# Optimization experiments

Measured on AMD Instinct MI355X. Metric: run time of the kernel, lower is better.

The kernel has to match this reference:

```python
import jax, jax.numpy as jnp
import numpy as np

DIM = 1024
H = 16
DH = DIM // H  # 64
B = 2
T = 2048
LEFT, RIGHT = 128, 128  # attention_window
CAUSAL = True
SCALE = 1.0 / float(np.sqrt(DH))


def rotate_half(x):
    x1, x2 = jnp.split(x, 2, axis=-1)
    return jnp.concatenate((-x2, x1), axis=-1)


def apply_rotary_pos_emb(pos, t):
    # pos: [b, t, dh] -> [b, 1, t, dh]; t: [b, h, t, dh]
    pos = pos[:, None]
    return t * jnp.cos(pos) + rotate_half(t) * jnp.sin(pos)


def setup_inputs() -> dict:
    key = jax.random.key(0)
    ks = jax.random.split(key, 6)
    s = 1.0 / np.sqrt(DIM)
    x = jax.random.normal(ks[0], (B, T, DIM), dtype=jnp.float32)
    attention_mask = jnp.ones((T, T), dtype=bool)
    rotary_emb = jax.random.normal(ks[1], (B, T, DH), dtype=jnp.float32)
    Wq = jax.random.normal(ks[2], (DIM, DIM), dtype=jnp.float32) * s
    Wk = jax.random.normal(ks[3], (DIM, DIM), dtype=jnp.float32) * s
    Wv = jax.random.normal(ks[4], (DIM, DIM), dtype=jnp.float32) * s
    Wo = jax.random.normal(ks[5], (DIM, DIM), dtype=jnp.float32) * s
    return {"x": x, "attention_mask": attention_mask, "rotary_emb": rotary_emb,
            "Wq": Wq, "Wk": Wk, "Wv": Wv, "Wo": Wo}


def _build_mask(attention_mask):
    # i = key/column index, j = query/row index (matches torch code)
    i = jnp.arange(T)[None, :]
    j = jnp.arange(T)[:, None]
    mask = (i >= j - LEFT) & (i <= j + RIGHT)  # sliding window
    if CAUSAL:
        mask = mask & (i <= j)  # tril
    return attention_mask & mask  # [T, T]


def reference(x, attention_mask, rotary_emb, Wq, Wk, Wv, Wo):
    b, t, d = x.shape
    # QKV projections (nn.Linear: x @ W.T), split heads: b t (h dh) -> b h t dh
    def proj(W):
        return (x @ W.T).reshape(b, t, H, DH).transpose(0, 2, 1, 3)
    q, k, v = proj(Wq), proj(Wk), proj(Wv)
    q = apply_rotary_pos_emb(rotary_emb, q)
    k = apply_rotary_pos_emb(rotary_emb, k)
    mask = _build_mask(attention_mask)  # [T, T]
    scores = jnp.einsum('bhqd,bhkd->bhqk', q, k) * SCALE
    neg = jnp.asarray(-1e9, scores.dtype)
    scores = jnp.where(mask, scores, neg)
    attn = jax.nn.softmax(scores, axis=-1)
    out = jnp.einsum('bhqk,bhkd->bhqd', attn, v)
    out = out.transpose(0, 2, 1, 3).reshape(b, t, d)  # b h t dh -> b t (h dh)
    return out @ Wo.T
```

## Files before the change

kernel.cpp:

```cpp
#include <hip/hip_runtime.h>
#include <hip/hip_bf16.h>
#include <cstdint>

#define DIMD 1024
#define NH 16
#define DHD 64
#define BB 2
#define TT 2048
#define MROWS (BB * TT)

typedef unsigned short u16;
typedef unsigned int u32;
typedef __attribute__((ext_vector_type(8))) __bf16 bf16x8;
typedef __attribute__((ext_vector_type(4))) float f32x4;

__device__ __forceinline__ float bf2f(u16 u) {
    union { unsigned int i; float f; } v; v.i = ((unsigned int)u) << 16; return v.f;
}
__device__ __forceinline__ u16 f2bf(float f) {
    union { float f; unsigned int i; } v; v.f = f;
    unsigned int u = v.i;
    unsigned int r = (u + 0x7fffu + ((u >> 16) & 1u)) >> 16;
    return (u16)r;
}
__device__ __forceinline__ int4 pack8(const float4& a, const float4& b) {
    union { int4 v; u16 u[8]; } t;
    t.u[0] = f2bf(a.x); t.u[1] = f2bf(a.y); t.u[2] = f2bf(a.z); t.u[3] = f2bf(a.w);
    t.u[4] = f2bf(b.x); t.u[5] = f2bf(b.y); t.u[6] = f2bf(b.z); t.u[7] = f2bf(b.w);
    return t.v;
}
__device__ __forceinline__ void gl_lds16(const u16* g, u16* l) {
    __builtin_amdgcn_global_load_lds(
        (const __attribute__((address_space(1))) u32*)g,
        (__attribute__((address_space(3))) u32*)l, 16, 0, 0);
}

__global__ __launch_bounds__(256) void convert_all(const float* __restrict__ x,
                                                   const float* __restrict__ Wq,
                                                   const float* __restrict__ Wk,
                                                   const float* __restrict__ Wv,
                                                   const float* __restrict__ Wo,
                                                   u16* __restrict__ xb,
                                                   u16* __restrict__ wqkv,
                                                   u16* __restrict__ wob) {
    int t = blockIdx.x * 256 + threadIdx.x;
    const float* src; u16* dst; int rel;
    if (t < 524288)      { src = x;  dst = xb;             rel = t; }
    else if (t < 655360) { src = Wq; dst = wqkv;           rel = t - 524288; }
    else if (t < 786432) { src = Wk; dst = wqkv + 1048576; rel = t - 655360; }
    else if (t < 917504) { src = Wv; dst = wqkv + 2097152; rel = t - 786432; }
    else                 { src = Wo; dst = wob;            rel = t - 917504; }
    size_t e = (size_t)rel * 8;
    float4 a = *(const float4*)(src + e);
    float4 b = *(const float4*)(src + e + 4);
    *(int4*)(dst + e) = pack8(a, b);
}

__global__ __launch_bounds__(256) void gemm_qkv(const u16* __restrict__ xb,
                                                const u16* __restrict__ wqkv,
                                                u16* __restrict__ qb,
                                                u16* __restrict__ kb,
                                                u16* __restrict__ vb,
                                                const float* __restrict__ rot) {
    constexpr int Kd = 1024;
    __shared__ u16 As[128 * 32];
    __shared__ u16 Bs[128 * 32];

    const int tid  = threadIdx.x;
    const int lane = tid & 63;
    const int w    = tid >> 6;
    const int m0   = blockIdx.y * 128;
    const int n0   = blockIdx.x * 128;

    const u16* Ag = xb   + (size_t)(m0 + 32 * w + (lane >> 2)) * Kd + (lane & 3) * 8;
    const u16* Bg = wqkv + (size_t)(n0 + 32 * w + (lane & 63) / 4) * Kd + (lane & 3) * 8;
    u16* Al0 = &As[(32 * w) * 32];
    u16* Al1 = &As[(32 * w + 16) * 32];
    u16* Bl0 = &Bs[(32 * w) * 32];
    u16* Bl1 = &Bs[(32 * w + 16) * 32];

    const int r16  = lane & 15;
    const int quad = lane >> 4;
    const int q8   = quad * 8;
    const int wm   = (w >> 1) * 64;
    const int wn   = (w & 1) * 64;

    f32x4 acc[4][4];
#pragma unroll
    for (int i = 0; i < 4; i++)
#pragma unroll
        for (int j = 0; j < 4; j++) acc[i][j] = f32x4{0.f, 0.f, 0.f, 0.f};

    for (int k0 = 0; k0 < Kd; k0 += 32) {
        __syncthreads();
        gl_lds16(Ag + k0, Al0);
        gl_lds16(Ag + 16 * Kd + k0, Al1);
        gl_lds16(Bg + k0, Bl0);
        gl_lds16(Bg + 16 * Kd + k0, Bl1);
        __syncthreads();

        bf16x8 af[4], bfr[4];
#pragma unroll
        for (int i = 0; i < 4; i++)
            af[i] = *(const bf16x8*)&As[(wm + i * 16 + r16) * 32 + q8];
#pragma unroll
        for (int j = 0; j < 4; j++)
            bfr[j] = *(const bf16x8*)&Bs[(wn + j * 16 + r16) * 32 + q8];
#pragma unroll
        for (int mi = 0; mi < 4; mi++)
#pragma unroll
            for (int ni = 0; ni < 4; ni++)
                acc[mi][ni] = __builtin_amdgcn_mfma_f32_16x16x32_bf16(
                    af[mi], bfr[ni], acc[mi][ni], 0, 0, 0);
    }

    const int wsel = n0 >> 10;
    const int nloc = (n0 & 1023) + wn;
    u16* C = (wsel == 0) ? qb : (wsel == 1) ? kb : vb;

    if (wsel < 2) {
#pragma unroll
        for (int mi = 0; mi < 4; mi++)
#pragma unroll
            for (int r = 0; r < 4; r++) {
                int row = m0 + wm + mi * 16 + quad * 4 + r;
#pragma unroll
                for (int ni = 0; ni < 2; ni++) {
                    int d = ni * 16 + r16;
                    float s0, c0, s1, c1;
                    __sincosf(rot[row * DHD + d], &s0, &c0);
                    __sincosf(rot[row * DHD + d + 32], &s1, &c1);
                    float x0 = acc[mi][ni][r], x1 = acc[mi][ni + 2][r];
                    C[(size_t)row * DIMD + nloc + d]      = f2bf(x0 * c0 - x1 * s0);
                    C[(size_t)row * DIMD + nloc + d + 32] = f2bf(x1 * c1 + x0 * s1);
                }
            }
    } else {
#pragma unroll
        for (int mi = 0; mi < 4; mi++)
#pragma unroll
            for (int ni = 0; ni < 4; ni++)
#pragma unroll
                for (int r = 0; r < 4; r++) {
                    int row = m0 + wm + mi * 16 + quad * 4 + r;
                    C[(size_t)row * DIMD + nloc + ni * 16 + r16] = f2bf(acc[mi][ni][r]);
                }
    }
}

__global__ __launch_bounds__(256) void gemm_out(const u16* __restrict__ A,
                                                const u16* __restrict__ Wb,
                                                float* __restrict__ C) {
    constexpr int Kd = 1024, Nd = 1024;
    __shared__ u16 As[64 * 32];
    __shared__ u16 Bs[128 * 32];

    const int tid  = threadIdx.x;
    const int lane = tid & 63;
    const int w    = tid >> 6;
    const int m0   = blockIdx.y * 64;
    const int n0   = blockIdx.x * 128;

    const u16* Ag = A  + (size_t)(m0 + 16 * w + (lane >> 2)) * Kd + (lane & 3) * 8;
    const u16* Bg = Wb + (size_t)(n0 + 32 * w + (lane >> 2)) * Kd + (lane & 3) * 8;
    u16* Al  = &As[(16 * w) * 32];
    u16* Bl0 = &Bs[(32 * w) * 32];
    u16* Bl1 = &Bs[(32 * w + 16) * 32];

    const int r16  = lane & 15;
    const int quad = lane >> 4;
    const int q8   = quad * 8;
    const int cb   = (w >> 1) * 64 + (w & 1) * 16;

    f32x4 acc[4][2];
#pragma unroll
    for (int i = 0; i < 4; i++)
#pragma unroll
        for (int j = 0; j < 2; j++) acc[i][j] = f32x4{0.f, 0.f, 0.f, 0.f};

    for (int k0 = 0; k0 < Kd; k0 += 32) {
        __syncthreads();
        gl_lds16(Ag + k0, Al);
        gl_lds16(Bg + k0, Bl0);
        gl_lds16(Bg + 16 * Kd + k0, Bl1);
        __syncthreads();

        bf16x8 af[4], bfr[2];
#pragma unroll
        for (int i = 0; i < 4; i++)
            af[i] = *(const bf16x8*)&As[(i * 16 + r16) * 32 + q8];
#pragma unroll
        for (int j = 0; j < 2; j++)
            bfr[j] = *(const bf16x8*)&Bs[(cb + j * 32 + r16) * 32 + q8];
#pragma unroll
        for (int mi = 0; mi < 4; mi++)
#pragma unroll
            for (int ni = 0; ni < 2; ni++)
                acc[mi][ni] = __builtin_amdgcn_mfma_f32_16x16x32_bf16(
                    af[mi], bfr[ni], acc[mi][ni], 0, 0, 0);
    }

#pragma unroll
    for (int mi = 0; mi < 4; mi++)
#pragma unroll
        for (int j = 0; j < 2; j++)
#pragma unroll
            for (int r = 0; r < 4; r++) {
                int row = m0 + mi * 16 + quad * 4 + r;
                C[(size_t)row * Nd + n0 + cb + j * 32 + r16] = acc[mi][j][r];
            }
}

__global__ __launch_bounds__(256) void attn_kernel(const u16* __restrict__ Q,
                                                   const u16* __restrict__ K,
                                                   const u16* __restrict__ V,
                                                   u16* __restrict__ O) {
    constexpr int LDK = 72;
    constexpr int LDV = 200;
    __shared__ u16 Ks[192 * LDK];
    __shared__ u16 Qs[64 * LDK];
    __shared__ u16 VTs[64 * LDV];

    const int tid = threadIdx.x;
    const int L   = tid & 63;
    const int w   = tid >> 6;
    const int b   = blockIdx.z;
    const int h   = blockIdx.y;
    const int q0  = blockIdx.x * 64;
    const int kstart = q0 - 128;

    for (int i = tid; i < 512; i += 256) {
        int qr = i >> 3, c = (i & 7) * 8;
        int t = q0 + qr;
        *(int4*)&Qs[qr * LDK + c] =
            *(const int4*)&Q[(size_t)(b * TT + t) * DIMD + h * DHD + c];
    }
    for (int i = tid; i < 1536; i += 256) {
        int kr = i >> 3, c = (i & 7) * 8;
        int kk = kstart + kr;
        int4 val = make_int4(0, 0, 0, 0);
        if (kk >= 0)
            val = *(const int4*)&K[(size_t)(b * TT + kk) * DIMD + h * DHD + c];
        *(int4*)&Ks[kr * LDK + c] = val;
    }
    for (int i = tid; i < 1536; i += 256) {
        int kr = i >> 3, c = (i & 7) * 8;
        int kk = kstart + kr;
        union { int4 v; u16 u[8]; } tmp;
        tmp.v = make_int4(0, 0, 0, 0);
        if (kk >= 0)
            tmp.v = *(const int4*)&V[(size_t)(b * TT + kk) * DIMD + h * DHD + c];
#pragma unroll
        for (int j = 0; j < 8; j++) VTs[(c + j) * LDV + kr] = tmp.u[j];
    }
    __syncthreads();

    const int r16  = L & 15;
    const int quad = L >> 4;
    const int q8   = quad * 8;

    bf16x8 aq0 = *(const bf16x8*)&Qs[(w * 16 + r16) * LDK + q8];
    bf16x8 aq1 = *(const bf16x8*)&Qs[(w * 16 + r16) * LDK + 32 + q8];

    float st[12][4];
    float rmax[4] = {-1e30f, -1e30f, -1e30f, -1e30f};
    const float SC = 0.125f;

#pragma unroll
    for (int kt = 0; kt < 12; kt++) {
        bf16x8 bk0 = *(const bf16x8*)&Ks[(kt * 16 + r16) * LDK + q8];
        bf16x8 bk1 = *(const bf16x8*)&Ks[(kt * 16 + r16) * LDK + 32 + q8];
        f32x4 s = f32x4{0.f, 0.f, 0.f, 0.f};
        s = __builtin_amdgcn_mfma_f32_16x16x32_bf16(aq0, bk0, s, 0, 0, 0);
        s = __builtin_amdgcn_mfma_f32_16x16x32_bf16(aq1, bk1, s, 0, 0, 0);
        int ka = kstart + kt * 16 + r16;
#pragma unroll
        for (int r = 0; r < 4; r++) {
            int qa = q0 + w * 16 + quad * 4 + r;
            float sv = s[r] * SC;
            bool ok = (ka >= 0) && (ka <= qa) && (ka >= qa - 128);
            sv = ok ? sv : -1e30f;
            st[kt][r] = sv;
            rmax[r] = fmaxf(rmax[r], sv);
        }
    }
#pragma unroll
    for (int off = 8; off >= 1; off >>= 1)
#pragma unroll
        for (int r = 0; r < 4; r++)
            rmax[r] = fmaxf(rmax[r], __shfl_xor(rmax[r], off, 64));

    __syncthreads();

    u16* Ps = &Ks[w * 16 * LDV];
    float rsum[4] = {0.f, 0.f, 0.f, 0.f};
#pragma unroll
    for (int kt = 0; kt < 12; kt++)
#pragma unroll
        for (int r = 0; r < 4; r++) {
            float p = __expf(st[kt][r] - rmax[r]);
            rsum[r] += p;
            Ps[(quad * 4 + r) * LDV + kt * 16 + r16] = f2bf(p);
        }
#pragma unroll
    for (int off = 8; off >= 1; off >>= 1)
#pragma unroll
        for (int r = 0; r < 4; r++)
            rsum[r] += __shfl_xor(rsum[r], off, 64);
    float rinv[4];
#pragma unroll
    for (int r = 0; r < 4; r++) rinv[r] = 1.0f / rsum[r];

    __syncthreads();

    bf16x8 pa[6];
#pragma unroll
    for (int kc = 0; kc < 6; kc++)
        pa[kc] = *(const bf16x8*)&Ps[r16 * LDV + kc * 32 + q8];

#pragma unroll
    for (int nt = 0; nt < 4; nt++) {
        f32x4 acc = f32x4{0.f, 0.f, 0.f, 0.f};
#pragma unroll
        for (int kc = 0; kc < 6; kc++) {
            bf16x8 bv = *(const bf16x8*)&VTs[(nt * 16 + r16) * LDV + kc * 32 + q8];
            acc = __builtin_amdgcn_mfma_f32_16x16x32_bf16(pa[kc], bv, acc, 0, 0, 0);
        }
#pragma unroll
        for (int r = 0; r < 4; r++) {
            int qa = q0 + w * 16 + quad * 4 + r;
            O[(size_t)(b * TT + qa) * DIMD + h * DHD + nt * 16 + r16] =
                f2bf(acc[r] * rinv[r]);
        }
    }
}

extern "C" void kernel_launch(void* const* d_in, const int* in_sizes, int n_in,
                              void* d_out, int out_size, void* d_ws, size_t ws_size,
                              hipStream_t stream) {
    const float* x   = (const float*)d_in[0];
    const float* rot = (const float*)d_in[2];
    const float* Wq  = (const float*)d_in[3];
    const float* Wk  = (const float*)d_in[4];
    const float* Wv  = (const float*)d_in[5];
    const float* Wo  = (const float*)d_in[6];
    float* out = (float*)d_out;

    u16* xb   = (u16*)d_ws;
    u16* wqkv = xb + 4194304;
    u16* wob  = wqkv + 3145728;
    u16* qb   = wob + 1048576;
    u16* kb   = qb + 4194304;
    u16* vb   = kb + 4194304;
    u16* ab   = vb + 4194304;

    convert_all<<<4096, 256, 0, stream>>>(x, Wq, Wk, Wv, Wo, xb, wqkv, wob);
    gemm_qkv<<<dim3(3 * DIMD / 128, MROWS / 128), 256, 0, stream>>>(
        xb, wqkv, qb, kb, vb, rot);
    attn_kernel<<<dim3(TT / 64, NH, BB), 256, 0, stream>>>(qb, kb, vb, ab);
    gemm_out<<<dim3(DIMD / 128, MROWS / 64), 256, 0, stream>>>(ab, wob, out);
}
```

Baseline: 185.4 us.

## Double-buffer LDS tiles in QKV and output projection GEMMs

Both GEMM kernels now keep two shared-memory buffers per operand and issue the global-to-LDS loads for the next K tile before computing on the current one, leaving one barrier per tile instead of two. The aim is to hide global load latency behind MFMA work. It doubles LDS use per block, which may lower occupancy. Correctness rests on gl_lds16 completion being ordered by the following __syncthreads; if that wait is missing, the compute step could read stale data.

```diff
diff --git a/kernel.cpp b/kernel.cpp
--- a/kernel.cpp
+++ b/kernel.cpp
@@ -63,8 +63,8 @@
                                                 u16* __restrict__ vb,
                                                 const float* __restrict__ rot) {
     constexpr int Kd = 1024;
-    __shared__ u16 As[128 * 32];
-    __shared__ u16 Bs[128 * 32];
+    __shared__ u16 As[2][128 * 32];
+    __shared__ u16 Bs[2][128 * 32];
 
     const int tid  = threadIdx.x;
     const int lane = tid & 63;
@@ -73,11 +73,9 @@
     const int n0   = blockIdx.x * 128;
 
     const u16* Ag = xb   + (size_t)(m0 + 32 * w + (lane >> 2)) * Kd + (lane & 3) * 8;
-    const u16* Bg = wqkv + (size_t)(n0 + 32 * w + (lane & 63) / 4) * Kd + (lane & 3) * 8;
-    u16* Al0 = &As[(32 * w) * 32];
-    u16* Al1 = &As[(32 * w + 16) * 32];
-    u16* Bl0 = &Bs[(32 * w) * 32];
-    u16* Bl1 = &Bs[(32 * w + 16) * 32];
+    const u16* Bg = wqkv + (size_t)(n0 + 32 * w + (lane >> 2)) * Kd + (lane & 3) * 8;
+    const int loff0 = (32 * w) * 32;
+    const int loff1 = (32 * w + 16) * 32;
 
     const int r16  = lane & 15;
     const int quad = lane >> 4;
@@ -91,27 +89,37 @@
 #pragma unroll
         for (int j = 0; j < 4; j++) acc[i][j] = f32x4{0.f, 0.f, 0.f, 0.f};
 
-    for (int k0 = 0; k0 < Kd; k0 += 32) {
-        __syncthreads();
-        gl_lds16(Ag + k0, Al0);
-        gl_lds16(Ag + 16 * Kd + k0, Al1);
-        gl_lds16(Bg + k0, Bl0);
-        gl_lds16(Bg + 16 * Kd + k0, Bl1);
-        __syncthreads();
-
+    auto stage = [&](int k, int buf) {
+        gl_lds16(Ag + k, &As[buf][loff0]);
+        gl_lds16(Ag + 16 * Kd + k, &As[buf][loff1]);
+        gl_lds16(Bg + k, &Bs[buf][loff0]);
+        gl_lds16(Bg + 16 * Kd + k, &Bs[buf][loff1]);
+    };
+    auto compute = [&](int buf) {
         bf16x8 af[4], bfr[4];
 #pragma unroll
         for (int i = 0; i < 4; i++)
-            af[i] = *(const bf16x8*)&As[(wm + i * 16 + r16) * 32 + q8];
+            af[i] = *(const bf16x8*)&As[buf][(wm + i * 16 + r16) * 32 + q8];
 #pragma unroll
         for (int j = 0; j < 4; j++)
-            bfr[j] = *(const bf16x8*)&Bs[(wn + j * 16 + r16) * 32 + q8];
+            bfr[j] = *(const bf16x8*)&Bs[buf][(wn + j * 16 + r16) * 32 + q8];
 #pragma unroll
         for (int mi = 0; mi < 4; mi++)
 #pragma unroll
             for (int ni = 0; ni < 4; ni++)
                 acc[mi][ni] = __builtin_amdgcn_mfma_f32_16x16x32_bf16(
                     af[mi], bfr[ni], acc[mi][ni], 0, 0, 0);
+    };
+
+    stage(0, 0);
+#pragma unroll 1
+    for (int k0 = 0; k0 < Kd; k0 += 64) {
+        __syncthreads();
+        if (k0 + 32 < Kd) stage(k0 + 32, 1);
+        compute(0);
+        __syncthreads();
+        if (k0 + 64 < Kd) stage(k0 + 64, 0);
+        compute(1);
     }
 
     const int wsel = n0 >> 10;
@@ -152,8 +160,8 @@
                                                 const u16* __restrict__ Wb,
                                                 float* __restrict__ C) {
     constexpr int Kd = 1024, Nd = 1024;
-    __shared__ u16 As[64 * 32];
-    __shared__ u16 Bs[128 * 32];
+    __shared__ u16 As[2][64 * 32];
+    __shared__ u16 Bs[2][128 * 32];
 
     const int tid  = threadIdx.x;
     const int lane = tid & 63;
@@ -163,9 +171,9 @@
 
     const u16* Ag = A  + (size_t)(m0 + 16 * w + (lane >> 2)) * Kd + (lane & 3) * 8;
     const u16* Bg = Wb + (size_t)(n0 + 32 * w + (lane >> 2)) * Kd + (lane & 3) * 8;
-    u16* Al  = &As[(16 * w) * 32];
-    u16* Bl0 = &Bs[(32 * w) * 32];
-    u16* Bl1 = &Bs[(32 * w + 16) * 32];
+    const int aoff  = (16 * w) * 32;
+    const int boff0 = (32 * w) * 32;
+    const int boff1 = (32 * w + 16) * 32;
 
     const int r16  = lane & 15;
     const int quad = lane >> 4;
@@ -178,26 +186,36 @@
 #pragma unroll
         for (int j = 0; j < 2; j++) acc[i][j] = f32x4{0.f, 0.f, 0.f, 0.f};
 
-    for (int k0 = 0; k0 < Kd; k0 += 32) {
-        __syncthreads();
-        gl_lds16(Ag + k0, Al);
-        gl_lds16(Bg + k0, Bl0);
-        gl_lds16(Bg + 16 * Kd + k0, Bl1);
-        __syncthreads();
-
+    auto stage = [&](int k, int buf) {
+        gl_lds16(Ag + k, &As[buf][aoff]);
+        gl_lds16(Bg + k, &Bs[buf][boff0]);
+        gl_lds16(Bg + 16 * Kd + k, &Bs[buf][boff1]);
+    };
+    auto compute = [&](int buf) {
         bf16x8 af[4], bfr[2];
 #pragma unroll
         for (int i = 0; i < 4; i++)
-            af[i] = *(const bf16x8*)&As[(i * 16 + r16) * 32 + q8];
+            af[i] = *(const bf16x8*)&As[buf][(i * 16 + r16) * 32 + q8];
 #pragma unroll
         for (int j = 0; j < 2; j++)
-            bfr[j] = *(const bf16x8*)&Bs[(cb + j * 32 + r16) * 32 + q8];
+            bfr[j] = *(const bf16x8*)&Bs[buf][(cb + j * 32 + r16) * 32 + q8];
 #pragma unroll
         for (int mi = 0; mi < 4; mi++)
 #pragma unroll
             for (int ni = 0; ni < 2; ni++)
                 acc[mi][ni] = __builtin_amdgcn_mfma_f32_16x16x32_bf16(
                     af[mi], bfr[ni], acc[mi][ni], 0, 0, 0);
+    };
+
+    stage(0, 0);
+#pragma unroll 1
+    for (int k0 = 0; k0 < Kd; k0 += 64) {
+        __syncthreads();
+        if (k0 + 32 < Kd) stage(k0 + 32, 1);
+        compute(0);
+        __syncthreads();
+        if (k0 + 64 < Kd) stage(k0 + 64, 0);
+        compute(1);
     }
 
 #pragma unroll
```

Result: slower. 191.5 us (+3.3%).

## Shrink QKV GEMM tile and stream attention K/V from global via pretransposed V

Applied to the files above, without the earlier changes.

The QKV GEMM tile drops from 128x128 to 128x64 and gets a higher occupancy hint, doubling the grid to fill more CUs. A separate kernel now transposes V once into head-major [d][t] layout. The attention kernel no longer stages Q, K and V in shared memory: it reads MFMA fragments straight from global (relying on cache) and uses LDS only for P. This removes a large LDS footprint and its barriers, but adds an extra kernel launch plus a V round trip, and leaves the attention loads uncoalesced.

```diff
diff --git a/kernel.cpp b/kernel.cpp
--- a/kernel.cpp
+++ b/kernel.cpp
@@ -14,9 +14,6 @@
 typedef __attribute__((ext_vector_type(8))) __bf16 bf16x8;
 typedef __attribute__((ext_vector_type(4))) float f32x4;
 
-__device__ __forceinline__ float bf2f(u16 u) {
-    union { unsigned int i; float f; } v; v.i = ((unsigned int)u) << 16; return v.f;
-}
 __device__ __forceinline__ u16 f2bf(float f) {
     union { float f; unsigned int i; } v; v.f = f;
     unsigned int u = v.i;
@@ -56,58 +53,56 @@
     *(int4*)(dst + e) = pack8(a, b);
 }
 
-__global__ __launch_bounds__(256) void gemm_qkv(const u16* __restrict__ xb,
-                                                const u16* __restrict__ wqkv,
-                                                u16* __restrict__ qb,
-                                                u16* __restrict__ kb,
-                                                u16* __restrict__ vb,
-                                                const float* __restrict__ rot) {
+__global__ __launch_bounds__(256, 6) void gemm_qkv(const u16* __restrict__ xb,
+                                                   const u16* __restrict__ wqkv,
+                                                   u16* __restrict__ qb,
+                                                   u16* __restrict__ kb,
+                                                   u16* __restrict__ vb,
+                                                   const float* __restrict__ rot) {
     constexpr int Kd = 1024;
     __shared__ u16 As[128 * 32];
-    __shared__ u16 Bs[128 * 32];
+    __shared__ u16 Bs[64 * 32];
 
     const int tid  = threadIdx.x;
     const int lane = tid & 63;
     const int w    = tid >> 6;
     const int m0   = blockIdx.y * 128;
-    const int n0   = blockIdx.x * 128;
+    const int n0   = blockIdx.x * 64;
 
     const u16* Ag = xb   + (size_t)(m0 + 32 * w + (lane >> 2)) * Kd + (lane & 3) * 8;
-    const u16* Bg = wqkv + (size_t)(n0 + 32 * w + (lane & 63) / 4) * Kd + (lane & 3) * 8;
+    const u16* Bg = wqkv + (size_t)(n0 + 16 * w + (lane >> 2)) * Kd + (lane & 3) * 8;
     u16* Al0 = &As[(32 * w) * 32];
     u16* Al1 = &As[(32 * w + 16) * 32];
-    u16* Bl0 = &Bs[(32 * w) * 32];
-    u16* Bl1 = &Bs[(32 * w + 16) * 32];
+    u16* Bl  = &Bs[(16 * w) * 32];
 
     const int r16  = lane & 15;
     const int quad = lane >> 4;
     const int q8   = quad * 8;
-    const int wm   = (w >> 1) * 64;
-    const int wn   = (w & 1) * 64;
-
-    f32x4 acc[4][4];
-#pragma unroll
-    for (int i = 0; i < 4; i++)
+    const int wm   = w * 32;
+
+    f32x4 acc[2][4];
+#pragma unroll
+    for (int i = 0; i < 2; i++)
 #pragma unroll
         for (int j = 0; j < 4; j++) acc[i][j] = f32x4{0.f, 0.f, 0.f, 0.f};
 
+#pragma unroll 1
     for (int k0 = 0; k0 < Kd; k0 += 32) {
         __syncthreads();
         gl_lds16(Ag + k0, Al0);
         gl_lds16(Ag + 16 * Kd + k0, Al1);
-        gl_lds16(Bg + k0, Bl0);
-        gl_lds16(Bg + 16 * Kd + k0, Bl1);
+        gl_lds16(Bg + k0, Bl);
         __syncthreads();
 
-        bf16x8 af[4], bfr[4];
-#pragma unroll
-        for (int i = 0; i < 4; i++)
+        bf16x8 af[2], bfr[4];
+#pragma unroll
+        for (int i = 0; i < 2; i++)
             af[i] = *(const bf16x8*)&As[(wm + i * 16 + r16) * 32 + q8];
 #pragma unroll
         for (int j = 0; j < 4; j++)
-            bfr[j] = *(const bf16x8*)&Bs[(wn + j * 16 + r16) * 32 + q8];
-#pragma unroll
-        for (int mi = 0; mi < 4; mi++)
+            bfr[j] = *(const bf16x8*)&Bs[(j * 16 + r16) * 32 + q8];
+#pragma unroll
+        for (int mi = 0; mi < 2; mi++)
 #pragma unroll
             for (int ni = 0; ni < 4; ni++)
                 acc[mi][ni] = __builtin_amdgcn_mfma_f32_16x16x32_bf16(
@@ -115,12 +110,12 @@
     }
 
     const int wsel = n0 >> 10;
-    const int nloc = (n0 & 1023) + wn;
+    const int nloc = n0 & 1023;
     u16* C = (wsel == 0) ? qb : (wsel == 1) ? kb : vb;
 
     if (wsel < 2) {
 #pragma unroll
-        for (int mi = 0; mi < 4; mi++)
+        for (int mi = 0; mi < 2; mi++)
 #pragma unroll
             for (int r = 0; r < 4; r++) {
                 int row = m0 + wm + mi * 16 + quad * 4 + r;
@@ -137,7 +132,7 @@
             }
     } else {
 #pragma unroll
-        for (int mi = 0; mi < 4; mi++)
+        for (int mi = 0; mi < 2; mi++)
 #pragma unroll
             for (int ni = 0; ni < 4; ni++)
 #pragma unroll
@@ -148,78 +143,40 @@
     }
 }
 
-__global__ __launch_bounds__(256) void gemm_out(const u16* __restrict__ A,
-                                                const u16* __restrict__ Wb,
-                                                float* __restrict__ C) {
-    constexpr int Kd = 1024, Nd = 1024;
-    __shared__ u16 As[64 * 32];
-    __shared__ u16 Bs[128 * 32];
-
-    const int tid  = threadIdx.x;
-    const int lane = tid & 63;
-    const int w    = tid >> 6;
-    const int m0   = blockIdx.y * 64;
-    const int n0   = blockIdx.x * 128;
-
-    const u16* Ag = A  + (size_t)(m0 + 16 * w + (lane >> 2)) * Kd + (lane & 3) * 8;
-    const u16* Bg = Wb + (size_t)(n0 + 32 * w + (lane >> 2)) * Kd + (lane & 3) * 8;
-    u16* Al  = &As[(16 * w) * 32];
-    u16* Bl0 = &Bs[(32 * w) * 32];
-    u16* Bl1 = &Bs[(32 * w + 16) * 32];
-
-    const int r16  = lane & 15;
-    const int quad = lane >> 4;
-    const int q8   = quad * 8;
-    const int cb   = (w >> 1) * 64 + (w & 1) * 16;
-
-    f32x4 acc[4][2];
-#pragma unroll
-    for (int i = 0; i < 4; i++)
-#pragma unroll
-        for (int j = 0; j < 2; j++) acc[i][j] = f32x4{0.f, 0.f, 0.f, 0.f};
-
-    for (int k0 = 0; k0 < Kd; k0 += 32) {
-        __syncthreads();
-        gl_lds16(Ag + k0, Al);
-        gl_lds16(Bg + k0, Bl0);
-        gl_lds16(Bg + 16 * Kd + k0, Bl1);
-        __syncthreads();
-
-        bf16x8 af[4], bfr[2];
-#pragma unroll
-        for (int i = 0; i < 4; i++)
-            af[i] = *(const bf16x8*)&As[(i * 16 + r16) * 32 + q8];
-#pragma unroll
-        for (int j = 0; j < 2; j++)
-            bfr[j] = *(const bf16x8*)&Bs[(cb + j * 32 + r16) * 32 + q8];
-#pragma unroll
-        for (int mi = 0; mi < 4; mi++)
-#pragma unroll
-            for (int ni = 0; ni < 2; ni++)
-                acc[mi][ni] = __builtin_amdgcn_mfma_f32_16x16x32_bf16(
-                    af[mi], bfr[ni], acc[mi][ni], 0, 0, 0);
-    }
-
-#pragma unroll
-    for (int mi = 0; mi < 4; mi++)
-#pragma unroll
-        for (int j = 0; j < 2; j++)
-#pragma unroll
-            for (int r = 0; r < 4; r++) {
-                int row = m0 + mi * 16 + quad * 4 + r;
-                C[(size_t)row * Nd + n0 + cb + j * 32 + r16] = acc[mi][j][r];
-            }
+__global__ __launch_bounds__(256) void transpose_v(const u16* __restrict__ vb,
+                                                   u16* __restrict__ vbT) {
+    __shared__ u16 Ls[64 * 65];
+    const int i  = threadIdx.x;
+    const int t0 = blockIdx.x * 64;
+    const int h  = blockIdx.y;
+    const int b  = blockIdx.z;
+#pragma unroll
+    for (int r = 0; r < 2; r++) {
+        int t = r * 32 + (i >> 3);
+        int c = (i & 7) * 8;
+        union { int4 v; u16 u[8]; } tmp;
+        tmp.v = *(const int4*)&vb[(size_t)(b * TT + t0 + t) * DIMD + h * DHD + c];
+#pragma unroll
+        for (int j = 0; j < 8; j++) Ls[t * 65 + c + j] = tmp.u[j];
+    }
+    __syncthreads();
+#pragma unroll
+    for (int r = 0; r < 2; r++) {
+        int d  = r * 32 + (i >> 3);
+        int tc = (i & 7) * 8;
+        union { int4 v; u16 u[8]; } tmp;
+#pragma unroll
+        for (int j = 0; j < 8; j++) tmp.u[j] = Ls[(tc + j) * 65 + d];
+        *(int4*)&vbT[((size_t)(b * NH + h) * DHD + d) * TT + t0 + tc] = tmp.v;
+    }
 }
 
 __global__ __launch_bounds__(256) void attn_kernel(const u16* __restrict__ Q,
                                                    const u16* __restrict__ K,
-                                                   const u16* __restrict__ V,
+                                                   const u16* __restrict__ vbT,
                                                    u16* __restrict__ O) {
-    constexpr int LDK = 72;
-    constexpr int LDV = 200;
-    __shared__ u16 Ks[192 * LDK];
-    __shared__ u16 Qs[64 * LDK];
-    __shared__ u16 VTs[64 * LDV];
+    constexpr int LDP = 200;
+    __shared__ u16 Ps[4 * 16 * LDP];
 
     const int tid = threadIdx.x;
     const int L   = tid & 63;
@@ -229,38 +186,13 @@
     const int q0  = blockIdx.x * 64;
     const int kstart = q0 - 128;
 
-    for (int i = tid; i < 512; i += 256) {
-        int qr = i >> 3, c = (i & 7) * 8;
-        int t = q0 + qr;
-        *(int4*)&Qs[qr * LDK + c] =
-            *(const int4*)&Q[(size_t)(b * TT + t) * DIMD + h * DHD + c];
-    }
-    for (int i = tid; i < 1536; i += 256) {
-        int kr = i >> 3, c = (i & 7) * 8;
-        int kk = kstart + kr;
-        int4 val = make_int4(0, 0, 0, 0);
-        if (kk >= 0)
-            val = *(const int4*)&K[(size_t)(b * TT + kk) * DIMD + h * DHD + c];
-        *(int4*)&Ks[kr * LDK + c] = val;
-    }
-    for (int i = tid; i < 1536; i += 256) {
-        int kr = i >> 3, c = (i & 7) * 8;
-        int kk = kstart + kr;
-        union { int4 v; u16 u[8]; } tmp;
-        tmp.v = make_int4(0, 0, 0, 0);
-        if (kk >= 0)
-            tmp.v = *(const int4*)&V[(size_t)(b * TT + kk) * DIMD + h * DHD + c];
-#pragma unroll
-        for (int j = 0; j < 8; j++) VTs[(c + j) * LDV + kr] = tmp.u[j];
-    }
-    __syncthreads();
-
     const int r16  = L & 15;
     const int quad = L >> 4;
     const int q8   = quad * 8;
 
-    bf16x8 aq0 = *(const bf16x8*)&Qs[(w * 16 + r16) * LDK + q8];
-    bf16x8 aq1 = *(const bf16x8*)&Qs[(w * 16 + r16) * LDK + 32 + q8];
+    const size_t qrow = (size_t)(b * TT + q0 + w * 16 + r16) * DIMD + h * DHD;
+    bf16x8 aq0 = *(const bf16x8*)&Q[qrow + q8];
+    bf16x8 aq1 = *(const bf16x8*)&Q[qrow + 32 + q8];
 
     float st[12][4];
     float rmax[4] = {-1e30f, -1e30f, -1e30f, -1e30f};
@@ -268,12 +200,14 @@
 
 #pragma unroll
     for (int kt = 0; kt < 12; kt++) {
-        bf16x8 bk0 = *(const bf16x8*)&Ks[(kt * 16 + r16) * LDK + q8];
-        bf16x8 bk1 = *(const bf16x8*)&Ks[(kt * 16 + r16) * LDK + 32 + q8];
+        int ka = kstart + kt * 16 + r16;
+        int kc = ka < 0 ? 0 : ka;
+        const size_t krow = (size_t)(b * TT + kc) * DIMD + h * DHD;
+        bf16x8 bk0 = *(const bf16x8*)&K[krow + q8];
+        bf16x8 bk1 = *(const bf16x8*)&K[krow + 32 + q8];
         f32x4 s = f32x4{0.f, 0.f, 0.f, 0.f};
         s = __builtin_amdgcn_mfma_f32_16x16x32_bf16(aq0, bk0, s, 0, 0, 0);
         s = __builtin_amdgcn_mfma_f32_16x16x32_bf16(aq1, bk1, s, 0, 0, 0);
-        int ka = kstart + kt * 16 + r16;
 #pragma unroll
         for (int r = 0; r < 4; r++) {
             int qa = q0 + w * 16 + quad * 4 + r;
@@ -290,9 +224,7 @@
         for (int r = 0; r < 4; r++)
             rmax[r] = fmaxf(rmax[r], __shfl_xor(rmax[r], off, 64));
 
-    __syncthreads();
-
-    u16* Ps = &Ks[w * 16 * LDV];
+    u16* Pw = &Ps[w * 16 * LDP];
     float rsum[4] = {0.f, 0.f, 0.f, 0.f};
 #pragma unroll
     for (int kt = 0; kt < 12; kt++)
@@ -300,7 +232,7 @@
         for (int r = 0; r < 4; r++) {
             float p = __expf(st[kt][r] - rmax[r]);
             rsum[r] += p;
-            Ps[(quad * 4 + r) * LDV + kt * 16 + r16] = f2bf(p);
+            Pw[(quad * 4 + r) * LDP + kt * 16 + r16] = f2bf(p);
         }
 #pragma unroll
     for (int off = 8; off >= 1; off >>= 1)
@@ -316,14 +248,18 @@
     bf16x8 pa[6];
 #pragma unroll
     for (int kc = 0; kc < 6; kc++)
-        pa[kc] = *(const bf16x8*)&Ps[r16 * LDV + kc * 32 + q8];
-
+        pa[kc] = *(const bf16x8*)&Pw[r16 * LDP + kc * 32 + q8];
+
+    const size_t vbase = (size_t)(b * NH + h) * DHD * TT;
 #pragma unroll
     for (int nt = 0; nt < 4; nt++) {
         f32x4 acc = f32x4{0.f, 0.f, 0.f, 0.f};
+        const size_t vrow = vbase + (size_t)(nt * 16 + r16) * TT;
 #pragma unroll
         for (int kc = 0; kc < 6; kc++) {
-            bf16x8 bv = *(const bf16x8*)&VTs[(nt * 16 + r16) * LDV + kc * 32 + q8];
+            int kcol = kstart + kc * 32 + q8;
+            if (kcol < 0) kcol = 0;
+            bf16x8 bv = *(const bf16x8*)&vbT[vrow + kcol];
             acc = __builtin_amdgcn_mfma_f32_16x16x32_bf16(pa[kc], bv, acc, 0, 0, 0);
         }
 #pragma unroll
@@ -333,6 +269,70 @@
                 f2bf(acc[r] * rinv[r]);
         }
     }
+}
+
+__global__ __launch_bounds__(256) void gemm_out(const u16* __restrict__ A,
+                                                const u16* __restrict__ Wb,
+                                                float* __restrict__ C) {
+    constexpr int Kd = 1024, Nd = 1024;
+    __shared__ u16 As[64 * 32];
+    __shared__ u16 Bs[128 * 32];
+
+    const int tid  = threadIdx.x;
+    const int lane = tid & 63;
+    const int w    = tid >> 6;
+    const int m0   = blockIdx.y * 64;
+    const int n0   = blockIdx.x * 128;
+
+    const u16* Ag = A  + (size_t)(m0 + 16 * w + (lane >> 2)) * Kd + (lane & 3) * 8;
+    const u16* Bg = Wb + (size_t)(n0 + 32 * w + (lane >> 2)) * Kd + (lane & 3) * 8;
+    u16* Al  = &As[(16 * w) * 32];
+    u16* Bl0 = &Bs[(32 * w) * 32];
+    u16* Bl1 = &Bs[(32 * w + 16) * 32];
+
+    const int r16  = lane & 15;
+    const int quad = lane >> 4;
+    const int q8   = quad * 8;
+    const int cb   = (w >> 1) * 64 + (w & 1) * 16;
+
+    f32x4 acc[4][2];
+#pragma unroll
+    for (int i = 0; i < 4; i++)
+#pragma unroll
+        for (int j = 0; j < 2; j++) acc[i][j] = f32x4{0.f, 0.f, 0.f, 0.f};
+
+#pragma unroll 1
+    for (int k0 = 0; k0 < Kd; k0 += 32) {
+        __syncthreads();
+        gl_lds16(Ag + k0, Al);
+        gl_lds16(Bg + k0, Bl0);
+        gl_lds16(Bg + 16 * Kd + k0, Bl1);
+        __syncthreads();
+
+        bf16x8 af[4], bfr[2];
+#pragma unroll
+        for (int i = 0; i < 4; i++)
+            af[i] = *(const bf16x8*)&As[(i * 16 + r16) * 32 + q8];
+#pragma unroll
+        for (int j = 0; j < 2; j++)
+            bfr[j] = *(const bf16x8*)&Bs[(cb + j * 32 + r16) * 32 + q8];
+#pragma unroll
+        for (int mi = 0; mi < 4; mi++)
+#pragma unroll
+            for (int ni = 0; ni < 2; ni++)
+                acc[mi][ni] = __builtin_amdgcn_mfma_f32_16x16x32_bf16(
+                    af[mi], bfr[ni], acc[mi][ni], 0, 0, 0);
+    }
+
+#pragma unroll
+    for (int mi = 0; mi < 4; mi++)
+#pragma unroll
+        for (int j = 0; j < 2; j++)
+#pragma unroll
+            for (int r = 0; r < 4; r++) {
+                int row = m0 + mi * 16 + quad * 4 + r;
+                C[(size_t)row * Nd + n0 + cb + j * 32 + r16] = acc[mi][j][r];
+            }
 }
 
 extern "C" void kernel_launch(void* const* d_in, const int* in_sizes, int n_in,
@@ -353,10 +353,12 @@
     u16* kb   = qb + 4194304;
     u16* vb   = kb + 4194304;
     u16* ab   = vb + 4194304;
+    u16* vbT  = ab + 4194304;
 
     convert_all<<<4096, 256, 0, stream>>>(x, Wq, Wk, Wv, Wo, xb, wqkv, wob);
-    gemm_qkv<<<dim3(3 * DIMD / 128, MROWS / 128), 256, 0, stream>>>(
+    gemm_qkv<<<dim3(3 * DIMD / 64, MROWS / 128), 256, 0, stream>>>(
         xb, wqkv, qb, kb, vb, rot);
-    attn_kernel<<<dim3(TT / 64, NH, BB), 256, 0, stream>>>(qb, kb, vb, ab);
+    transpose_v<<<dim3(TT / 64, NH, BB), 256, 0, stream>>>(vb, vbT);
+    attn_kernel<<<dim3(TT / 64, NH, BB), 256, 0, stream>>>(qb, kb, vbT, ab);
     gemm_out<<<dim3(DIMD / 128, MROWS / 64), 256, 0, stream>>>(ab, wob, out);
 }
```

Result: slower. 198.4 us (+7.0%).

## Store V transposed from QKV GEMM and deepen GEMM K-step to 64

Applied to the files above, without the earlier changes.

The QKV GEMM epilogue now writes V in a per-head transposed layout [b,h,d,t], so the attention kernel can load V^T into shared memory with vector 16-byte copies instead of a scalar element-wise transpose. The QKV GEMM main loop also loads two 32-wide K slices per barrier pair, which halves the number of synchronisations. The cost is scattered 2-byte global stores in the V epilogue and twice the LDS use in the GEMM, which may reduce occupancy.

```diff
diff --git a/kernel.cpp b/kernel.cpp
--- a/kernel.cpp
+++ b/kernel.cpp
@@ -14,9 +14,6 @@
 typedef __attribute__((ext_vector_type(8))) __bf16 bf16x8;
 typedef __attribute__((ext_vector_type(4))) float f32x4;
 
-__device__ __forceinline__ float bf2f(u16 u) {
-    union { unsigned int i; float f; } v; v.i = ((unsigned int)u) << 16; return v.f;
-}
 __device__ __forceinline__ u16 f2bf(float f) {
     union { float f; unsigned int i; } v; v.f = f;
     unsigned int u = v.i;
@@ -60,11 +57,11 @@
                                                 const u16* __restrict__ wqkv,
                                                 u16* __restrict__ qb,
                                                 u16* __restrict__ kb,
-                                                u16* __restrict__ vb,
+                                                u16* __restrict__ vbT,
                                                 const float* __restrict__ rot) {
     constexpr int Kd = 1024;
-    __shared__ u16 As[128 * 32];
-    __shared__ u16 Bs[128 * 32];
+    __shared__ u16 As[2][128 * 32];
+    __shared__ u16 Bs[2][128 * 32];
 
     const int tid  = threadIdx.x;
     const int lane = tid & 63;
@@ -73,11 +70,9 @@
     const int n0   = blockIdx.x * 128;
 
     const u16* Ag = xb   + (size_t)(m0 + 32 * w + (lane >> 2)) * Kd + (lane & 3) * 8;
-    const u16* Bg = wqkv + (size_t)(n0 + 32 * w + (lane & 63) / 4) * Kd + (lane & 3) * 8;
-    u16* Al0 = &As[(32 * w) * 32];
-    u16* Al1 = &As[(32 * w + 16) * 32];
-    u16* Bl0 = &Bs[(32 * w) * 32];
-    u16* Bl1 = &Bs[(32 * w + 16) * 32];
+    const u16* Bg = wqkv + (size_t)(n0 + 32 * w + (lane >> 2)) * Kd + (lane & 3) * 8;
+    const int loff0 = (32 * w) * 32;
+    const int loff1 = (32 * w + 16) * 32;
 
     const int r16  = lane & 15;
     const int quad = lane >> 4;
@@ -91,34 +86,42 @@
 #pragma unroll
         for (int j = 0; j < 4; j++) acc[i][j] = f32x4{0.f, 0.f, 0.f, 0.f};
 
-    for (int k0 = 0; k0 < Kd; k0 += 32) {
+#pragma unroll 1
+    for (int k0 = 0; k0 < Kd; k0 += 64) {
         __syncthreads();
-        gl_lds16(Ag + k0, Al0);
-        gl_lds16(Ag + 16 * Kd + k0, Al1);
-        gl_lds16(Bg + k0, Bl0);
-        gl_lds16(Bg + 16 * Kd + k0, Bl1);
+        gl_lds16(Ag + k0, &As[0][loff0]);
+        gl_lds16(Ag + 16 * Kd + k0, &As[0][loff1]);
+        gl_lds16(Bg + k0, &Bs[0][loff0]);
+        gl_lds16(Bg + 16 * Kd + k0, &Bs[0][loff1]);
+        gl_lds16(Ag + k0 + 32, &As[1][loff0]);
+        gl_lds16(Ag + 16 * Kd + k0 + 32, &As[1][loff1]);
+        gl_lds16(Bg + k0 + 32, &Bs[1][loff0]);
+        gl_lds16(Bg + 16 * Kd + k0 + 32, &Bs[1][loff1]);
         __syncthreads();
 
-        bf16x8 af[4], bfr[4];
-#pragma unroll
-        for (int i = 0; i < 4; i++)
-            af[i] = *(const bf16x8*)&As[(wm + i * 16 + r16) * 32 + q8];
-#pragma unroll
-        for (int j = 0; j < 4; j++)
-            bfr[j] = *(const bf16x8*)&Bs[(wn + j * 16 + r16) * 32 + q8];
-#pragma unroll
-        for (int mi = 0; mi < 4; mi++)
-#pragma unroll
-            for (int ni = 0; ni < 4; ni++)
-                acc[mi][ni] = __builtin_amdgcn_mfma_f32_16x16x32_bf16(
-                    af[mi], bfr[ni], acc[mi][ni], 0, 0, 0);
+#pragma unroll
+        for (int p = 0; p < 2; p++) {
+            bf16x8 af[4], bfr[4];
+#pragma unroll
+            for (int i = 0; i < 4; i++)
+                af[i] = *(const bf16x8*)&As[p][(wm + i * 16 + r16) * 32 + q8];
+#pragma unroll
+            for (int j = 0; j < 4; j++)
+                bfr[j] = *(const bf16x8*)&Bs[p][(wn + j * 16 + r16) * 32 + q8];
+#pragma unroll
+            for (int mi = 0; mi < 4; mi++)
+#pragma unroll
+                for (int ni = 0; ni < 4; ni++)
+                    acc[mi][ni] = __builtin_amdgcn_mfma_f32_16x16x32_bf16(
+                        af[mi], bfr[ni], acc[mi][ni], 0, 0, 0);
+        }
     }
 
     const int wsel = n0 >> 10;
     const int nloc = (n0 & 1023) + wn;
-    u16* C = (wsel == 0) ? qb : (wsel == 1) ? kb : vb;
 
     if (wsel < 2) {
+        u16* C = (wsel == 0) ? qb : kb;
 #pragma unroll
         for (int mi = 0; mi < 4; mi++)
 #pragma unroll
@@ -143,77 +146,20 @@
 #pragma unroll
                 for (int r = 0; r < 4; r++) {
                     int row = m0 + wm + mi * 16 + quad * 4 + r;
-                    C[(size_t)row * DIMD + nloc + ni * 16 + r16] = f2bf(acc[mi][ni][r]);
+                    int b   = row >> 11;
+                    int t   = row & (TT - 1);
+                    int col = nloc + ni * 16 + r16;
+                    int h   = col >> 6;
+                    int d   = col & 63;
+                    vbT[((size_t)(b * NH + h) * DHD + d) * TT + t] =
+                        f2bf(acc[mi][ni][r]);
                 }
     }
-}
-
-__global__ __launch_bounds__(256) void gemm_out(const u16* __restrict__ A,
-                                                const u16* __restrict__ Wb,
-                                                float* __restrict__ C) {
-    constexpr int Kd = 1024, Nd = 1024;
-    __shared__ u16 As[64 * 32];
-    __shared__ u16 Bs[128 * 32];
-
-    const int tid  = threadIdx.x;
-    const int lane = tid & 63;
-    const int w    = tid >> 6;
-    const int m0   = blockIdx.y * 64;
-    const int n0   = blockIdx.x * 128;
-
-    const u16* Ag = A  + (size_t)(m0 + 16 * w + (lane >> 2)) * Kd + (lane & 3) * 8;
-    const u16* Bg = Wb + (size_t)(n0 + 32 * w + (lane >> 2)) * Kd + (lane & 3) * 8;
-    u16* Al  = &As[(16 * w) * 32];
-    u16* Bl0 = &Bs[(32 * w) * 32];
-    u16* Bl1 = &Bs[(32 * w + 16) * 32];
-
-    const int r16  = lane & 15;
-    const int quad = lane >> 4;
-    const int q8   = quad * 8;
-    const int cb   = (w >> 1) * 64 + (w & 1) * 16;
-
-    f32x4 acc[4][2];
-#pragma unroll
-    for (int i = 0; i < 4; i++)
-#pragma unroll
-        for (int j = 0; j < 2; j++) acc[i][j] = f32x4{0.f, 0.f, 0.f, 0.f};
-
-    for (int k0 = 0; k0 < Kd; k0 += 32) {
-        __syncthreads();
-        gl_lds16(Ag + k0, Al);
-        gl_lds16(Bg + k0, Bl0);
-        gl_lds16(Bg + 16 * Kd + k0, Bl1);
-        __syncthreads();
-
-        bf16x8 af[4], bfr[2];
-#pragma unroll
-        for (int i = 0; i < 4; i++)
-            af[i] = *(const bf16x8*)&As[(i * 16 + r16) * 32 + q8];
-#pragma unroll
-        for (int j = 0; j < 2; j++)
-            bfr[j] = *(const bf16x8*)&Bs[(cb + j * 32 + r16) * 32 + q8];
-#pragma unroll
-        for (int mi = 0; mi < 4; mi++)
-#pragma unroll
-            for (int ni = 0; ni < 2; ni++)
-                acc[mi][ni] = __builtin_amdgcn_mfma_f32_16x16x32_bf16(
-                    af[mi], bfr[ni], acc[mi][ni], 0, 0, 0);
-    }
-
-#pragma unroll
-    for (int mi = 0; mi < 4; mi++)
-#pragma unroll
-        for (int j = 0; j < 2; j++)
-#pragma unroll
-            for (int r = 0; r < 4; r++) {
-                int row = m0 + mi * 16 + quad * 4 + r;
-                C[(size_t)row * Nd + n0 + cb + j * 32 + r16] = acc[mi][j][r];
-            }
 }
 
 __global__ __launch_bounds__(256) void attn_kernel(const u16* __restrict__ Q,
                                                    const u16* __restrict__ K,
-                                                   const u16* __restrict__ V,
+                                                   const u16* __restrict__ vbT,
                                                    u16* __restrict__ O) {
     constexpr int LDK = 72;
     constexpr int LDV = 200;
@@ -231,9 +177,8 @@
 
     for (int i = tid; i < 512; i += 256) {
         int qr = i >> 3, c = (i & 7) * 8;
-        int t = q0 + qr;
         *(int4*)&Qs[qr * LDK + c] =
-            *(const int4*)&Q[(size_t)(b * TT + t) * DIMD + h * DHD + c];
+            *(const int4*)&Q[(size_t)(b * TT + q0 + qr) * DIMD + h * DHD + c];
     }
     for (int i = tid; i < 1536; i += 256) {
         int kr = i >> 3, c = (i & 7) * 8;
@@ -244,14 +189,13 @@
         *(int4*)&Ks[kr * LDK + c] = val;
     }
     for (int i = tid; i < 1536; i += 256) {
-        int kr = i >> 3, c = (i & 7) * 8;
-        int kk = kstart + kr;
-        union { int4 v; u16 u[8]; } tmp;
-        tmp.v = make_int4(0, 0, 0, 0);
+        int d = i / 24;
+        int c = (i % 24) * 8;
+        int kk = kstart + c;
+        int4 val = make_int4(0, 0, 0, 0);
         if (kk >= 0)
-            tmp.v = *(const int4*)&V[(size_t)(b * TT + kk) * DIMD + h * DHD + c];
-#pragma unroll
-        for (int j = 0; j < 8; j++) VTs[(c + j) * LDV + kr] = tmp.u[j];
+            val = *(const int4*)&vbT[((size_t)(b * NH + h) * DHD + d) * TT + kk];
+        *(int4*)&VTs[d * LDV + c] = val;
     }
     __syncthreads();
 
@@ -333,6 +277,70 @@
                 f2bf(acc[r] * rinv[r]);
         }
     }
+}
+
+__global__ __launch_bounds__(256) void gemm_out(const u16* __restrict__ A,
+                                                const u16* __restrict__ Wb,
+                                                float* __restrict__ C) {
+    constexpr int Kd = 1024, Nd = 1024;
+    __shared__ u16 As[64 * 32];
+    __shared__ u16 Bs[128 * 32];
+
+    const int tid  = threadIdx.x;
+    const int lane = tid & 63;
+    const int w    = tid >> 6;
+    const int m0   = blockIdx.y * 64;
+    const int n0   = blockIdx.x * 128;
+
+    const u16* Ag = A  + (size_t)(m0 + 16 * w + (lane >> 2)) * Kd + (lane & 3) * 8;
+    const u16* Bg = Wb + (size_t)(n0 + 32 * w + (lane >> 2)) * Kd + (lane & 3) * 8;
+    u16* Al  = &As[(16 * w) * 32];
+    u16* Bl0 = &Bs[(32 * w) * 32];
+    u16* Bl1 = &Bs[(32 * w + 16) * 32];
+
+    const int r16  = lane & 15;
+    const int quad = lane >> 4;
+    const int q8   = quad * 8;
+    const int cb   = (w >> 1) * 64 + (w & 1) * 16;
+
+    f32x4 acc[4][2];
+#pragma unroll
+    for (int i = 0; i < 4; i++)
+#pragma unroll
+        for (int j = 0; j < 2; j++) acc[i][j] = f32x4{0.f, 0.f, 0.f, 0.f};
+
+#pragma unroll 1
+    for (int k0 = 0; k0 < Kd; k0 += 32) {
+        __syncthreads();
+        gl_lds16(Ag + k0, Al);
+        gl_lds16(Bg + k0, Bl0);
+        gl_lds16(Bg + 16 * Kd + k0, Bl1);
+        __syncthreads();
+
+        bf16x8 af[4], bfr[2];
+#pragma unroll
+        for (int i = 0; i < 4; i++)
+            af[i] = *(const bf16x8*)&As[(i * 16 + r16) * 32 + q8];
+#pragma unroll
+        for (int j = 0; j < 2; j++)
+            bfr[j] = *(const bf16x8*)&Bs[(cb + j * 32 + r16) * 32 + q8];
+#pragma unroll
+        for (int mi = 0; mi < 4; mi++)
+#pragma unroll
+            for (int ni = 0; ni < 2; ni++)
+                acc[mi][ni] = __builtin_amdgcn_mfma_f32_16x16x32_bf16(
+                    af[mi], bfr[ni], acc[mi][ni], 0, 0, 0);
+    }
+
+#pragma unroll
+    for (int mi = 0; mi < 4; mi++)
+#pragma unroll
+        for (int j = 0; j < 2; j++)
+#pragma unroll
+            for (int r = 0; r < 4; r++) {
+                int row = m0 + mi * 16 + quad * 4 + r;
+                C[(size_t)row * Nd + n0 + cb + j * 32 + r16] = acc[mi][j][r];
+            }
 }
 
 extern "C" void kernel_launch(void* const* d_in, const int* in_sizes, int n_in,
@@ -351,12 +359,12 @@
     u16* wob  = wqkv + 3145728;
     u16* qb   = wob + 1048576;
     u16* kb   = qb + 4194304;
-    u16* vb   = kb + 4194304;
-    u16* ab   = vb + 4194304;
+    u16* vbT  = kb + 4194304;
+    u16* ab   = vbT + 4194304;
 
     convert_all<<<4096, 256, 0, stream>>>(x, Wq, Wk, Wv, Wo, xb, wqkv, wob);
     gemm_qkv<<<dim3(3 * DIMD / 128, MROWS / 128), 256, 0, stream>>>(
-        xb, wqkv, qb, kb, vb, rot);
-    attn_kernel<<<dim3(TT / 64, NH, BB), 256, 0, stream>>>(qb, kb, vb, ab);
+        xb, wqkv, qb, kb, vbT, rot);
+    attn_kernel<<<dim3(TT / 64, NH, BB), 256, 0, stream>>>(qb, kb, vbT, ab);
     gemm_out<<<dim3(DIMD / 128, MROWS / 64), 256, 0, stream>>>(ab, wob, out);
 }
```

After: 189.4 us. 1.02x slower.
